# Optimization experiments

Hardware: AMD Instinct MI355X
Metric: run time of the kernel (lower is better)

Reference implementation:

```python
import jax, jax.numpy as jnp
import numpy as np

DIM = 2048
N_HEADS = 32
N_KV_HEADS = 8
HEAD_DIM = 64
ROPE_BASE = 10000.0
BATCH = 2
SEQ = 2048


def apply_rope(x, cos, sin):
    # x: (B, S, H, hd); cos/sin: (1, S, 1, hd//2). Interleaved rotation.
    x1 = x[..., ::2]
    x2 = x[..., 1::2]
    r1 = x1 * cos - x2 * sin
    r2 = x1 * sin + x2 * cos
    return jnp.stack([r1, r2], axis=-1).reshape(x.shape)


def setup_inputs() -> dict:
    key = jax.random.key(0)
    ks = jax.random.split(key, 8)
    s = DIM ** -0.5
    x = jax.random.normal(ks[0], (BATCH, SEQ, DIM), dtype=jnp.float32)
    Wq = jax.random.normal(ks[1], (DIM, N_HEADS * HEAD_DIM), dtype=jnp.float32) * s
    Wk = jax.random.normal(ks[2], (DIM, N_KV_HEADS * HEAD_DIM), dtype=jnp.float32) * s
    Wv = jax.random.normal(ks[3], (DIM, N_KV_HEADS * HEAD_DIM), dtype=jnp.float32) * s
    bv = jax.random.normal(ks[4], (N_KV_HEADS * HEAD_DIM,), dtype=jnp.float32) * 0.01
    Wo = jax.random.normal(ks[5], (N_HEADS * HEAD_DIM, DIM), dtype=jnp.float32) * s
    bo = jax.random.normal(ks[6], (DIM,), dtype=jnp.float32) * 0.01
    # causal mask: 1 where attended, 0 where masked
    mask = jnp.tril(jnp.ones((SEQ, SEQ), dtype=jnp.int32))[None, None]
    return {"x": x, "Wq": Wq, "Wk": Wk, "Wv": Wv, "bv": bv, "Wo": Wo, "bo": bo, "mask": mask}


def reference(x, Wq, Wk, Wv, bv, Wo, bo, mask):
    B, S, _ = x.shape
    q = (x @ Wq).reshape(B, S, N_HEADS, HEAD_DIM)
    k = (x @ Wk).reshape(B, S, N_KV_HEADS, HEAD_DIM)
    v = (x @ Wv + bv).reshape(B, S, N_KV_HEADS, HEAD_DIM)

    # RoPE tables
    theta = 1.0 / ROPE_BASE ** (jnp.arange(0, HEAD_DIM, 2, dtype=jnp.float32) / HEAD_DIM)
    freqs = jnp.arange(S, dtype=jnp.float32)[:, None] * theta[None, :]  # (S, hd/2)
    cos = jnp.cos(freqs)[None, :, None, :]
    sin = jnp.sin(freqs)[None, :, None, :]

    q = apply_rope(q, cos, sin)
    k = apply_rope(k, cos, sin)

    rf = N_HEADS // N_KV_HEADS
    k = jnp.repeat(k, rf, axis=2)  # materialized GQA repeat, as in source
    v = jnp.repeat(v, rf, axis=2)

    scale = HEAD_DIM ** -0.5
    scores = jnp.einsum("bqhd,bkhd->bhqk", q, k) * scale  # (B, H, S, S)
    scores = jnp.where(mask == 0, -jnp.inf, scores)
    attn = jax.nn.softmax(scores, axis=-1)
    out = jnp.einsum("bhqk,bkhd->bqhd", attn, v).reshape(B, S, N_HEADS * HEAD_DIM)
    return out @ Wo + bo
```

## Files before the change

kernel.cpp:

```cpp
#include <hip/hip_runtime.h>
#include <hip/hip_bf16.h>

#define DIMX     2048
#define N_HEADS  32
#define N_KVH    8
#define HEAD_D   64
#define BATCH    2
#define SEQ      2048
#define M_ROWS   (BATCH * SEQ)
#define QKVN     3072
#define THETA_C  0.2878231366242557f
#define C1SCALE  0.1803368801111204f

typedef __attribute__((ext_vector_type(8))) short short8;
typedef __attribute__((ext_vector_type(4))) float f32x4;

#define DEV static __device__ __forceinline__

DEV float b2f(unsigned short u) { return __uint_as_float(((unsigned int)u) << 16); }
DEV unsigned short f2b(float f) {
  unsigned int x = __float_as_uint(f);
  return (unsigned short)((x + 0x7fffu + ((x >> 16) & 1u)) >> 16);
}
DEV void gld16(const void* g, void* lds) {
  __builtin_amdgcn_global_load_lds(
      (const __attribute__((address_space(1))) unsigned int*)g,
      (__attribute__((address_space(3))) unsigned int*)lds, 16, 0, 0);
}

__global__ void cast_k(const float* __restrict__ s, unsigned short* __restrict__ d, int n8)
{
  int i = blockIdx.x * 256 + threadIdx.x;
  if (i >= n8) return;
  float4 a = ((const float4*)s)[i * 2];
  float4 b = ((const float4*)s)[i * 2 + 1];
  short8 o;
  o[0] = (short)f2b(a.x); o[1] = (short)f2b(a.y);
  o[2] = (short)f2b(a.z); o[3] = (short)f2b(a.w);
  o[4] = (short)f2b(b.x); o[5] = (short)f2b(b.y);
  o[6] = (short)f2b(b.z); o[7] = (short)f2b(b.w);
  ((short8*)d)[i] = o;
}

__global__ __launch_bounds__(256) void transcast_k(
    const float* __restrict__ W, unsigned short* __restrict__ Wt, int Kd, int N)
{
  __shared__ float tile[64][65];
  const int t = threadIdx.x;
  const int k0 = blockIdx.y * 64, n0 = blockIdx.x * 64;
  const int r = t >> 4, c4 = (t & 15) << 2;
  #pragma unroll
  for (int pp = 0; pp < 4; ++pp) {
    float4 v = *(const float4*)(W + (size_t)(k0 + pp * 16 + r) * N + n0 + c4);
    *(float4*)&tile[pp * 16 + r][c4] = v;
  }
  __syncthreads();
  const int n = t >> 2, kc = (t & 3) << 4;
  short8 u0, u1;
  #pragma unroll
  for (int j = 0; j < 8; ++j) u0[j] = (short)f2b(tile[kc + j][n]);
  #pragma unroll
  for (int j = 0; j < 8; ++j) u1[j] = (short)f2b(tile[kc + 8 + j][n]);
  unsigned short* dst = Wt + (size_t)(n0 + n) * Kd + k0 + kc;
  *(short8*)dst = u0;
  *(short8*)(dst + 8) = u1;
}

#define TM 128
#define TK 32

template<int OUTB>
__global__ __launch_bounds__(256) void gemm_bf16_k(
    const unsigned short* __restrict__ A,
    const unsigned short* __restrict__ Bt,
    const float* __restrict__ bias,
    void* __restrict__ Cp, int M, int N, int K)
{
  __shared__ unsigned short Al[TM * TK];
  __shared__ unsigned short Bl[TM * TK];
  const int t = threadIdx.x;
  const int l = t & 63, w = t >> 6;
  const int col = l & 15, grp = l >> 4;
  const int wr = (w >> 1) * 64, wc = (w & 1) * 64;
  const int bm = blockIdx.y * 128, bn = blockIdx.x * 128;

  f32x4 acc[4][4];
  #pragma unroll
  for (int mi = 0; mi < 4; ++mi)
    #pragma unroll
    for (int ni = 0; ni < 4; ++ni) acc[mi][ni] = (f32x4){0.f, 0.f, 0.f, 0.f};

  const int lr = l >> 2;
  const int lc = (l & 3) * 8;
  const unsigned short* Aw = A + (size_t)(bm + w * 32 + lr) * K + lc;
  const unsigned short* Bw = Bt + (size_t)(bn + w * 32 + lr) * K + lc;
  unsigned short* Ald = &Al[(w * 32) * TK];
  unsigned short* Bld = &Bl[(w * 32) * TK];

  for (int k0 = 0; k0 < K; k0 += TK) {
    __syncthreads();
    gld16(Aw + k0, Ald);
    gld16(Aw + (size_t)16 * K + k0, Ald + 16 * TK);
    gld16(Bw + k0, Bld);
    gld16(Bw + (size_t)16 * K + k0, Bld + 16 * TK);
    __syncthreads();
    short8 af[4], bf[4];
    #pragma unroll
    for (int mi = 0; mi < 4; ++mi)
      af[mi] = *(const short8*)&Al[(wr + mi * 16 + col) * TK + grp * 8];
    #pragma unroll
    for (int ni = 0; ni < 4; ++ni)
      bf[ni] = *(const short8*)&Bl[(wc + ni * 16 + col) * TK + grp * 8];
    #pragma unroll
    for (int mi = 0; mi < 4; ++mi)
      #pragma unroll
      for (int ni = 0; ni < 4; ++ni)
        acc[mi][ni] = __builtin_amdgcn_mfma_f32_16x16x32_bf16(af[mi], bf[ni], acc[mi][ni], 0, 0, 0);
  }

  #pragma unroll
  for (int ni = 0; ni < 4; ++ni) {
    const int cn = bn + wc + ni * 16 + col;
    const float bvv = bias ? bias[cn] : 0.f;
    #pragma unroll
    for (int mi = 0; mi < 4; ++mi) {
      #pragma unroll
      for (int i = 0; i < 4; ++i) {
        const int cm = bm + wr + mi * 16 + grp * 4 + i;
        const float v = acc[mi][ni][i] + bvv;
        if (OUTB) ((unsigned short*)Cp)[(size_t)cm * N + cn] = f2b(v);
        else      ((float*)Cp)[(size_t)cm * N + cn] = v;
      }
    }
  }
}

__global__ void rope_b_k(unsigned short* __restrict__ qkv)
{
  int i = blockIdx.x * 256 + threadIdx.x;
  unsigned short* p; int row, c8; float osc;
  if (i < M_ROWS * 256) {
    row = i >> 8; c8 = i & 255; osc = C1SCALE;
    p = qkv + (size_t)row * QKVN + c8 * 8;
  } else {
    i -= M_ROWS * 256;
    if (i >= M_ROWS * 64) return;
    row = i >> 6; c8 = i & 63; osc = 1.0f;
    p = qkv + (size_t)row * QKVN + 2048 + c8 * 8;
  }
  const int s = row & (SEQ - 1);
  const int j0 = (c8 & 7) * 4;
  short8 v = *(short8*)p;
  short8 o;
  #pragma unroll
  for (int pp = 0; pp < 4; ++pp) {
    float th = __expf(-(float)(j0 + pp) * THETA_C);
    float ang = (float)s * th;
    float sn, cs;
    sincosf(ang, &sn, &cs);
    float x1 = b2f((unsigned short)v[2 * pp]);
    float x2 = b2f((unsigned short)v[2 * pp + 1]);
    o[2 * pp]     = (short)f2b((x1 * cs - x2 * sn) * osc);
    o[2 * pp + 1] = (short)f2b((x1 * sn + x2 * cs) * osc);
  }
  *(short8*)p = o;
}

__global__ __launch_bounds__(256) void vt_cast_k(
    const unsigned short* __restrict__ qkv, const float* __restrict__ bv,
    unsigned short* __restrict__ vt)
{
  __shared__ unsigned short tile[64][72];
  const int t = threadIdx.x;
  const int s0 = blockIdx.x * 64, kvh = blockIdx.y, b = blockIdx.z;
  const int r = t >> 3, c = (t & 7) * 8;
  #pragma unroll
  for (int pp = 0; pp < 2; ++pp) {
    short8 vv = *(const short8*)(qkv + (size_t)(b * SEQ + s0 + r + pp * 32) * QKVN + 2560 + kvh * 64 + c);
    short8 ov;
    #pragma unroll
    for (int j = 0; j < 8; ++j)
      ov[j] = (short)f2b(b2f((unsigned short)vv[j]) + bv[kvh * 64 + c + j]);
    *(short8*)&tile[r + pp * 32][c] = ov;
  }
  __syncthreads();
  const int d = t >> 2, sc = (t & 3) * 16;
  short8 u0, u1;
  #pragma unroll
  for (int j = 0; j < 8; ++j) u0[j] = (short)tile[sc + j][d];
  #pragma unroll
  for (int j = 0; j < 8; ++j) u1[j] = (short)tile[sc + 8 + j][d];
  unsigned short* dst = vt + (size_t)((b * N_KVH + kvh) * 64 + d) * SEQ + s0 + sc;
  *(short8*)dst = u0;
  *(short8*)(dst + 8) = u1;
}

__global__ __launch_bounds__(256) void attn_mfma_k(
    const unsigned short* __restrict__ qkv,
    const unsigned short* __restrict__ vt,
    unsigned short* __restrict__ ob)
{
  __shared__ unsigned short P[4][32][72];
  const int t = threadIdx.x, l = t & 63, w = t >> 6;
  const int col = l & 15, grp = l >> 4;
  const int h = blockIdx.x, b = blockIdx.y;
  const int pairid = blockIdx.z * 4 + w;
  const int kvh = h >> 2;

  const unsigned short* kbase = qkv + (size_t)(b * SEQ) * QKVN + 2048 + kvh * 64;
  const unsigned short* vbase = vt + (size_t)((b * N_KVH + kvh) * 64) * SEQ;

  #pragma unroll
  for (int half = 0; half < 2; ++half) {
    const int strip = half ? (63 - pairid) : pairid;
    const int qr = strip * 32;

    short8 aq[2][2];
    #pragma unroll
    for (int j = 0; j < 2; ++j) {
      const unsigned short* qrow = qkv + (size_t)(b * SEQ + qr + j * 16 + col) * QKVN + h * 64;
      aq[j][0] = *(const short8*)(qrow + grp * 8);
      aq[j][1] = *(const short8*)(qrow + 32 + grp * 8);
    }

    f32x4 o[2][4];
    #pragma unroll
    for (int j = 0; j < 2; ++j)
      #pragma unroll
      for (int ti = 0; ti < 4; ++ti) o[j][ti] = (f32x4){0.f, 0.f, 0.f, 0.f};
    float ls[8];
    #pragma unroll
    for (int i = 0; i < 8; ++i) ls[i] = 0.f;

    const int wkend = qr + 32;

    for (int kt = 0; kt < wkend; kt += 64) {
      short8 kreg[8], vreg[8];
      #pragma unroll
      for (int ti = 0; ti < 4; ++ti) {
        const unsigned short* kr = kbase + (size_t)(kt + ti * 16 + col) * QKVN;
        kreg[ti * 2 + 0] = *(const short8*)(kr + grp * 8);
        kreg[ti * 2 + 1] = *(const short8*)(kr + 32 + grp * 8);
      }
      #pragma unroll
      for (int ti = 0; ti < 4; ++ti) {
        const unsigned short* vr = vbase + (size_t)(ti * 16 + col) * SEQ + kt + grp * 8;
        vreg[ti * 2 + 0] = *(const short8*)(vr);
        vreg[ti * 2 + 1] = *(const short8*)(vr + 32);
      }

      f32x4 sc[2][4];
      #pragma unroll
      for (int ti = 0; ti < 4; ++ti) {
        #pragma unroll
        for (int j = 0; j < 2; ++j) {
          f32x4 s = (f32x4){0.f, 0.f, 0.f, 0.f};
          s = __builtin_amdgcn_mfma_f32_16x16x32_bf16(aq[j][0], kreg[ti * 2 + 0], s, 0, 0, 0);
          s = __builtin_amdgcn_mfma_f32_16x16x32_bf16(aq[j][1], kreg[ti * 2 + 1], s, 0, 0, 0);
          sc[j][ti] = s;
        }
      }

      const bool diag = (kt + 32 >= qr);
      #pragma unroll
      for (int j = 0; j < 2; ++j) {
        #pragma unroll
        for (int i = 0; i < 4; ++i) {
          const int qg = qr + j * 16 + grp * 4 + i;
          float a0 = sc[j][0][i], a1 = sc[j][1][i], a2 = sc[j][2][i], a3 = sc[j][3][i];
          if (diag) {
            if (kt +  0 + col > qg) a0 = -1e30f;
            if (kt + 16 + col > qg) a1 = -1e30f;
            if (kt + 32 + col > qg) a2 = -1e30f;
            if (kt + 48 + col > qg) a3 = -1e30f;
          }
          float p0 = exp2f(a0), p1 = exp2f(a1);
          float p2 = exp2f(a2), p3 = exp2f(a3);
          ls[j * 4 + i] += (p0 + p1) + (p2 + p3);
          const int pr = j * 16 + grp * 4 + i;
          P[w][pr][ 0 + col] = f2b(p0);
          P[w][pr][16 + col] = f2b(p1);
          P[w][pr][32 + col] = f2b(p2);
          P[w][pr][48 + col] = f2b(p3);
        }
      }

      #pragma unroll
      for (int kh = 0; kh < 2; ++kh) {
        short8 pa[2];
        #pragma unroll
        for (int j = 0; j < 2; ++j)
          pa[j] = *(const short8*)&P[w][j * 16 + col][kh * 32 + grp * 8];
        #pragma unroll
        for (int ti = 0; ti < 4; ++ti)
          #pragma unroll
          for (int j = 0; j < 2; ++j)
            o[j][ti] = __builtin_amdgcn_mfma_f32_16x16x32_bf16(pa[j], vreg[ti * 2 + kh], o[j][ti], 0, 0, 0);
      }
    }

    float inv[8];
    #pragma unroll
    for (int i = 0; i < 8; ++i) {
      float s = ls[i];
      #pragma unroll
      for (int off = 1; off < 16; off <<= 1) s += __shfl_xor(s, off);
      inv[i] = 1.0f / s;
    }

    #pragma unroll
    for (int j = 0; j < 2; ++j) {
      unsigned short* orow = ob + (size_t)(b * SEQ + qr + j * 16 + grp * 4) * 2048 + h * 64;
      #pragma unroll
      for (int ti = 0; ti < 4; ++ti)
        #pragma unroll
        for (int i = 0; i < 4; ++i)
          orow[(size_t)i * 2048 + ti * 16 + col] = f2b(o[j][ti][i] * inv[j * 4 + i]);
    }
  }
}

extern "C" void kernel_launch(void* const* d_in, const int* in_sizes, int n_in,
                              void* d_out, int out_size, void* d_ws, size_t ws_size,
                              hipStream_t stream)
{
  const float* x  = (const float*)d_in[0];
  const float* Wq = (const float*)d_in[1];
  const float* Wk = (const float*)d_in[2];
  const float* Wv = (const float*)d_in[3];
  const float* bv = (const float*)d_in[4];
  const float* Wo = (const float*)d_in[5];
  const float* bo = (const float*)d_in[6];
  float* out = (float*)d_out;

  unsigned short* p = (unsigned short*)d_ws;
  unsigned short* xb   = p; p += (size_t)M_ROWS * DIMX;
  unsigned short* Wqkt = p; p += (size_t)QKVN * DIMX;
  unsigned short* Wot  = p; p += (size_t)DIMX * DIMX;
  unsigned short* qkv  = p; p += (size_t)M_ROWS * QKVN;
  unsigned short* vtb  = p; p += (size_t)M_ROWS * 512;
  unsigned short* ab = xb;

  cast_k<<<4096, 256, 0, stream>>>(x, xb, M_ROWS * DIMX / 8);
  transcast_k<<<dim3(32, 32), 256, 0, stream>>>(Wq, Wqkt,                     DIMX, 2048);
  transcast_k<<<dim3(8, 32),  256, 0, stream>>>(Wk, Wqkt + (size_t)2048 * DIMX, DIMX, 512);
  transcast_k<<<dim3(8, 32),  256, 0, stream>>>(Wv, Wqkt + (size_t)2560 * DIMX, DIMX, 512);
  transcast_k<<<dim3(32, 32), 256, 0, stream>>>(Wo, Wot,                      DIMX, 2048);

  gemm_bf16_k<1><<<dim3(QKVN / 128, M_ROWS / 128), 256, 0, stream>>>(
      xb, Wqkt, nullptr, qkv, M_ROWS, QKVN, DIMX);

  rope_b_k<<<5120, 256, 0, stream>>>(qkv);
  vt_cast_k<<<dim3(32, 8, 2), 256, 0, stream>>>(qkv, bv, vtb);

  attn_mfma_k<<<dim3(N_HEADS, BATCH, 8), 256, 0, stream>>>(qkv, vtb, ab);

  gemm_bf16_k<0><<<dim3(DIMX / 128, M_ROWS / 128), 256, 0, stream>>>(
      ab, Wot, bo, out, M_ROWS, DIMX, DIMX);
}
```

Before: 400.1 us.

## Pack bf16 conversions, precompute RoPE table, swizzle GEMM blocks, vectorize P stores

Replaces the scalar float-to-bf16 rounding with packed two-wide conversions in the cast, transpose, RoPE and attention kernels. RoPE now reads cos/sin from a precomputed table built by a new small kernel instead of calling exp and sincos per element. The GEMM remaps block indices so that consecutive blocks spread across the chiplet-like partitions, aiming for better L2 reuse. In attention, the probability tile is written with one 8-byte store per row by permuting key order in P, and the V transpose is permuted to match; this cuts LDS store count but relies on the two permutations staying consistent.

```diff
diff --git a/kernel.cpp b/kernel.cpp
--- a/kernel.cpp
+++ b/kernel.cpp
@@ -22,24 +22,38 @@
   unsigned int x = __float_as_uint(f);
   return (unsigned short)((x + 0x7fffu + ((x >> 16) & 1u)) >> 16);
 }
+DEV unsigned int pk2(float lo, float hi) {
+  __hip_bfloat162 h = __float22bfloat162_rn(make_float2(lo, hi));
+  unsigned int u;
+  __builtin_memcpy(&u, &h, 4);
+  return u;
+}
 DEV void gld16(const void* g, void* lds) {
   __builtin_amdgcn_global_load_lds(
       (const __attribute__((address_space(1))) unsigned int*)g,
       (__attribute__((address_space(3))) unsigned int*)lds, 16, 0, 0);
 }
 
+__global__ void tab_k(float2* __restrict__ tab)
+{
+  int i = blockIdx.x * 256 + threadIdx.x;
+  int s = i >> 5, j = i & 31;
+  float th = __expf(-(float)j * THETA_C);
+  float sn, cs;
+  sincosf((float)s * th, &sn, &cs);
+  tab[i] = make_float2(cs, sn);
+}
+
 __global__ void cast_k(const float* __restrict__ s, unsigned short* __restrict__ d, int n8)
 {
   int i = blockIdx.x * 256 + threadIdx.x;
   if (i >= n8) return;
   float4 a = ((const float4*)s)[i * 2];
   float4 b = ((const float4*)s)[i * 2 + 1];
-  short8 o;
-  o[0] = (short)f2b(a.x); o[1] = (short)f2b(a.y);
-  o[2] = (short)f2b(a.z); o[3] = (short)f2b(a.w);
-  o[4] = (short)f2b(b.x); o[5] = (short)f2b(b.y);
-  o[6] = (short)f2b(b.z); o[7] = (short)f2b(b.w);
-  ((short8*)d)[i] = o;
+  uint4 o;
+  o.x = pk2(a.x, a.y); o.y = pk2(a.z, a.w);
+  o.z = pk2(b.x, b.y); o.w = pk2(b.z, b.w);
+  ((uint4*)d)[i] = o;
 }
 
 __global__ __launch_bounds__(256) void transcast_k(
@@ -56,14 +70,18 @@
   }
   __syncthreads();
   const int n = t >> 2, kc = (t & 3) << 4;
-  short8 u0, u1;
-  #pragma unroll
-  for (int j = 0; j < 8; ++j) u0[j] = (short)f2b(tile[kc + j][n]);
-  #pragma unroll
-  for (int j = 0; j < 8; ++j) u1[j] = (short)f2b(tile[kc + 8 + j][n]);
+  uint4 u0, u1;
+  u0.x = pk2(tile[kc + 0][n], tile[kc + 1][n]);
+  u0.y = pk2(tile[kc + 2][n], tile[kc + 3][n]);
+  u0.z = pk2(tile[kc + 4][n], tile[kc + 5][n]);
+  u0.w = pk2(tile[kc + 6][n], tile[kc + 7][n]);
+  u1.x = pk2(tile[kc + 8][n], tile[kc + 9][n]);
+  u1.y = pk2(tile[kc + 10][n], tile[kc + 11][n]);
+  u1.z = pk2(tile[kc + 12][n], tile[kc + 13][n]);
+  u1.w = pk2(tile[kc + 14][n], tile[kc + 15][n]);
   unsigned short* dst = Wt + (size_t)(n0 + n) * Kd + k0 + kc;
-  *(short8*)dst = u0;
-  *(short8*)(dst + 8) = u1;
+  *(uint4*)dst = u0;
+  *(uint4*)(dst + 8) = u1;
 }
 
 #define TM 128
@@ -82,7 +100,11 @@
   const int l = t & 63, w = t >> 6;
   const int col = l & 15, grp = l >> 4;
   const int wr = (w >> 1) * 64, wc = (w & 1) * 64;
-  const int bm = blockIdx.y * 128, bn = blockIdx.x * 128;
+
+  const int gx = gridDim.x;
+  const int lin = blockIdx.y * gx + blockIdx.x;
+  const int wg = (lin & 7) * ((gx * gridDim.y) >> 3) + (lin >> 3);
+  const int bm = (wg / gx) * 128, bn = (wg % gx) * 128;
 
   f32x4 acc[4][4];
   #pragma unroll
@@ -135,7 +157,7 @@
   }
 }
 
-__global__ void rope_b_k(unsigned short* __restrict__ qkv)
+__global__ void rope_b_k(unsigned short* __restrict__ qkv, const float2* __restrict__ tab)
 {
   int i = blockIdx.x * 256 + threadIdx.x;
   unsigned short* p; int row, c8; float osc;
@@ -151,19 +173,17 @@
   const int s = row & (SEQ - 1);
   const int j0 = (c8 & 7) * 4;
   short8 v = *(short8*)p;
-  short8 o;
+  uint4 o;
+  unsigned int ou[4];
   #pragma unroll
   for (int pp = 0; pp < 4; ++pp) {
-    float th = __expf(-(float)(j0 + pp) * THETA_C);
-    float ang = (float)s * th;
-    float sn, cs;
-    sincosf(ang, &sn, &cs);
+    float2 cs = tab[(s << 5) + j0 + pp];
     float x1 = b2f((unsigned short)v[2 * pp]);
     float x2 = b2f((unsigned short)v[2 * pp + 1]);
-    o[2 * pp]     = (short)f2b((x1 * cs - x2 * sn) * osc);
-    o[2 * pp + 1] = (short)f2b((x1 * sn + x2 * cs) * osc);
-  }
-  *(short8*)p = o;
+    ou[pp] = pk2((x1 * cs.x - x2 * cs.y) * osc, (x1 * cs.y + x2 * cs.x) * osc);
+  }
+  o.x = ou[0]; o.y = ou[1]; o.z = ou[2]; o.w = ou[3];
+  *(uint4*)p = o;
 }
 
 __global__ __launch_bounds__(256) void vt_cast_k(
@@ -187,9 +207,11 @@
   const int d = t >> 2, sc = (t & 3) * 16;
   short8 u0, u1;
   #pragma unroll
-  for (int j = 0; j < 8; ++j) u0[j] = (short)tile[sc + j][d];
-  #pragma unroll
-  for (int j = 0; j < 8; ++j) u1[j] = (short)tile[sc + 8 + j][d];
+  for (int j = 0; j < 8; ++j) {
+    const int p0 = sc + j, p1 = sc + 8 + j;
+    u0[j] = (short)tile[(p0 & 3) * 16 + (p0 >> 2)][d];
+    u1[j] = (short)tile[(p1 & 3) * 16 + (p1 >> 2)][d];
+  }
   unsigned short* dst = vt + (size_t)((b * N_KVH + kvh) * 64 + d) * SEQ + s0 + sc;
   *(short8*)dst = u0;
   *(short8*)(dst + 8) = u1;
@@ -277,11 +299,10 @@
           float p0 = exp2f(a0), p1 = exp2f(a1);
           float p2 = exp2f(a2), p3 = exp2f(a3);
           ls[j * 4 + i] += (p0 + p1) + (p2 + p3);
-          const int pr = j * 16 + grp * 4 + i;
-          P[w][pr][ 0 + col] = f2b(p0);
-          P[w][pr][16 + col] = f2b(p1);
-          P[w][pr][32 + col] = f2b(p2);
-          P[w][pr][48 + col] = f2b(p3);
+          uint2 u;
+          u.x = pk2(p0, p1);
+          u.y = pk2(p2, p3);
+          *(uint2*)&P[w][j * 16 + grp * 4 + i][col * 4] = u;
         }
       }
 
@@ -339,18 +360,20 @@
   unsigned short* Wot  = p; p += (size_t)DIMX * DIMX;
   unsigned short* qkv  = p; p += (size_t)M_ROWS * QKVN;
   unsigned short* vtb  = p; p += (size_t)M_ROWS * 512;
+  float2* tab = (float2*)p;  p += (size_t)SEQ * 32 * 4;
   unsigned short* ab = xb;
 
+  tab_k<<<256, 256, 0, stream>>>(tab);
   cast_k<<<4096, 256, 0, stream>>>(x, xb, M_ROWS * DIMX / 8);
-  transcast_k<<<dim3(32, 32), 256, 0, stream>>>(Wq, Wqkt,                     DIMX, 2048);
+  transcast_k<<<dim3(32, 32), 256, 0, stream>>>(Wq, Wqkt,                       DIMX, 2048);
   transcast_k<<<dim3(8, 32),  256, 0, stream>>>(Wk, Wqkt + (size_t)2048 * DIMX, DIMX, 512);
   transcast_k<<<dim3(8, 32),  256, 0, stream>>>(Wv, Wqkt + (size_t)2560 * DIMX, DIMX, 512);
-  transcast_k<<<dim3(32, 32), 256, 0, stream>>>(Wo, Wot,                      DIMX, 2048);
+  transcast_k<<<dim3(32, 32), 256, 0, stream>>>(Wo, Wot,                        DIMX, 2048);
 
   gemm_bf16_k<1><<<dim3(QKVN / 128, M_ROWS / 128), 256, 0, stream>>>(
       xb, Wqkt, nullptr, qkv, M_ROWS, QKVN, DIMX);
 
-  rope_b_k<<<5120, 256, 0, stream>>>(qkv);
+  rope_b_k<<<5120, 256, 0, stream>>>(qkv, tab);
   vt_cast_k<<<dim3(32, 8, 2), 256, 0, stream>>>(qkv, bv, vtb);
 
   attn_mfma_k<<<dim3(N_HEADS, BATCH, 8), 256, 0, stream>>>(qkv, vtb, ab);
```

Measured after the change: 398.5 us. About the same (-0.4%).
